# Performance work log

Hardware: AMD Instinct MI355X
Metric: run time of the kernel (lower is better)

Reference implementation:

```python
import jax, jax.numpy as jnp
import numpy as np

D = 1024       # embedding_dim
H = 16         # num_attention_heads
B = 2
S = 2048       # seq_len == context_len


def setup_inputs() -> dict:
    key = jax.random.key(0)
    k1, k2, k3 = jax.random.split(key, 3)
    X = jax.random.normal(k1, (B, S, D), dtype=jnp.float32)
    W_qkv = jax.random.normal(k2, (D, 3 * D), dtype=jnp.float32) * 0.02
    b_qkv = jnp.zeros((3 * D,), dtype=jnp.float32)
    W_out = jax.random.normal(k3, (D, D), dtype=jnp.float32) * 0.02
    b_out = jnp.zeros((D,), dtype=jnp.float32)
    return {"X": X, "W_qkv": W_qkv, "b_qkv": b_qkv, "W_out": W_out, "b_out": b_out}


def reference(X, W_qkv, b_qkv, W_out, b_out):
    b, s, d = X.shape
    hd = d // H
    # fused QKV projection (GPT-2 Conv1D == x @ W + b)
    qkv = X @ W_qkv + b_qkv                       # [b, s, 3d]
    q, k, v = jnp.split(qkv, 3, axis=2)
    # [b, h, s, hd]
    q = q.reshape(b, s, H, hd).transpose(0, 2, 1, 3)
    k = k.reshape(b, s, H, hd).transpose(0, 2, 1, 3)
    v = v.reshape(b, s, H, hd).transpose(0, 2, 1, 3)
    # NOTE: source scales by rsqrt(embedding_dim), not head_dim
    scale = 1.0 / jnp.sqrt(jnp.float32(d))
    scores = jnp.einsum("bhqd,bhkd->bhqk", q, k) * scale
    causal = jnp.tril(jnp.ones((s, s), dtype=bool))
    scores = jnp.where(causal[None, None], scores, -jnp.inf)
    # attention_dropout applied pre-softmax in source; identity at eval (p used here = 0)
    probs = jax.nn.softmax(scores, axis=-1)
    attn = jnp.einsum("bhqk,bhkd->bhqd", probs, v)
    attn = attn.transpose(0, 2, 1, 3).reshape(b, s, d)
    out = attn @ W_out + b_out                    # outwards proj; dropout eval = identity
    return out
```

## Files before the change

kernel.cpp:

```cpp
#include <hip/hip_runtime.h>

#define S_LEN 2048
#define DIM   1024
#define NHEAD 16
#define HDIM  64
#define Q_PRESCALE 0.045084220027780106f

typedef __attribute__((ext_vector_type(8))) short  short8;
typedef __attribute__((ext_vector_type(4))) float  floatx4;
typedef __attribute__((ext_vector_type(4))) unsigned short ushort4v;
typedef __attribute__((ext_vector_type(4))) unsigned int uintx4;

__device__ inline unsigned short f2bf(float f) {
  unsigned v = __builtin_bit_cast(unsigned, f);
  v += 0x7FFFu + ((v >> 16) & 1u);
  return (unsigned short)(v >> 16);
}

__device__ inline unsigned cvt_pk_bf16(float a, float b) {
  unsigned r;
  asm("v_cvt_pk_bf16_f32 %0, %1, %2" : "=v"(r) : "v"(a), "v"(b));
  return r;
}

__device__ inline void permlane16_swap_rw(unsigned &a, unsigned &b) {
  asm("v_permlane16_swap_b32 %0, %1" : "+v"(a), "+v"(b));
}

__device__ inline void async16(const unsigned short* g, unsigned short* l) {
  __builtin_amdgcn_global_load_lds(
      (const __attribute__((address_space(1))) unsigned int*)g,
      (__attribute__((address_space(3))) unsigned int*)l, 16, 0, 0);
}

__global__ __launch_bounds__(256) void prep_kernel(
    const float* __restrict__ X, const float* __restrict__ Wqkv,
    const float* __restrict__ Wout, unsigned short* __restrict__ Xb,
    unsigned short* __restrict__ Wqkvt, unsigned short* __restrict__ Woutt) {
  const int j = blockIdx.x, t = threadIdx.x;
  if (j >= 4096) {
    int i = ((j - 4096) * 256 + t) * 8;
    float4 a = *(const float4*)&X[i];
    float4 b = *(const float4*)&X[i + 4];
    short8 o;
    o[0] = (short)f2bf(a.x); o[1] = (short)f2bf(a.y);
    o[2] = (short)f2bf(a.z); o[3] = (short)f2bf(a.w);
    o[4] = (short)f2bf(b.x); o[5] = (short)f2bf(b.y);
    o[6] = (short)f2bf(b.z); o[7] = (short)f2bf(b.w);
    *(short8*)&Xb[i] = o;
    return;
  }
  __shared__ unsigned short tile[32][33];
  const float* in; unsigned short* out; int N, tn, tk;
  if (j < 3072) { in = Wqkv; out = Wqkvt; N = 3072; tn = j % 96; tk = j / 96; }
  else { int u = j - 3072; in = Wout; out = Woutt; N = 1024; tn = u & 31; tk = u >> 5; }
  const int n0 = tn * 32, k0 = tk * 32;
  const int tx = t & 31, ty = t >> 5;
#pragma unroll
  for (int i = 0; i < 32; i += 8)
    tile[ty + i][tx] = f2bf(in[(size_t)(k0 + ty + i) * N + n0 + tx]);
  __syncthreads();
#pragma unroll
  for (int i = 0; i < 32; i += 8)
    out[(size_t)(n0 + ty + i) * 1024 + k0 + tx] = tile[tx][ty + i];
}

#define GEMM128_BODY(APTR, BPTR)                                                   \
  __shared__ __align__(16) unsigned short As[128][64];                             \
  __shared__ __align__(16) unsigned short Bs[128][64];                             \
  const int m0 = blockIdx.y * 128, n0 = blockIdx.x * 128;                          \
  const int t = threadIdx.x, lane = t & 63, wave = t >> 6;                         \
  const int quad = lane >> 4, l16 = lane & 15;                                     \
  const int wm = (wave >> 1) * 64, wn = (wave & 1) * 64;                           \
  const int lr = lane >> 3, lc = lane & 7, sc8 = (lc ^ lr) * 8;                    \
  const int sw = l16 & 7;                                                          \
  const int pA0 = (quad ^ sw) * 8, pA1 = ((4 + quad) ^ sw) * 8;                    \
  floatx4 acc[4][4];                                                               \
  _Pragma("unroll") for (int mi = 0; mi < 4; mi++)                                 \
      _Pragma("unroll") for (int ni = 0; ni < 4; ni++)                             \
          acc[mi][ni] = (floatx4){0.f, 0.f, 0.f, 0.f};                             \
  for (int k0 = 0; k0 < DIM; k0 += 64) {                                           \
    _Pragma("unroll") for (int i = 0; i < 4; i++) {                                \
      int rb = wave * 32 + i * 8;                                                  \
      async16(&APTR[(size_t)(m0 + rb + lr) * DIM + k0 + sc8], &As[rb][0]);         \
      async16(&BPTR[(size_t)(n0 + rb + lr) * DIM + k0 + sc8], &Bs[rb][0]);         \
    }                                                                              \
    __syncthreads();                                                               \
    short8 a0[4], a1[4];                                                           \
    _Pragma("unroll") for (int mi = 0; mi < 4; mi++) {                             \
      int row = wm + mi * 16 + l16;                                                \
      a0[mi] = *(const short8*)&As[row][pA0];                                      \
      a1[mi] = *(const short8*)&As[row][pA1];                                      \
    }                                                                              \
    _Pragma("unroll") for (int ni = 0; ni < 4; ni++) {                             \
      int row = wn + ni * 16 + l16;                                                \
      short8 b0 = *(const short8*)&Bs[row][pA0];                                   \
      short8 b1 = *(const short8*)&Bs[row][pA1];                                   \
      _Pragma("unroll") for (int mi = 0; mi < 4; mi++) {                           \
        acc[mi][ni] = __builtin_amdgcn_mfma_f32_16x16x32_bf16(a0[mi], b0, acc[mi][ni], 0, 0, 0); \
        acc[mi][ni] = __builtin_amdgcn_mfma_f32_16x16x32_bf16(a1[mi], b1, acc[mi][ni], 0, 0, 0); \
      }                                                                            \
    }                                                                              \
    __syncthreads();                                                               \
  }

__global__ __launch_bounds__(256) void gemm_qkv128(
    const unsigned short* __restrict__ Xb,
    const unsigned short* __restrict__ Wt,
    const float* __restrict__ bias,
    unsigned short* __restrict__ Qg,
    unsigned short* __restrict__ Kg,
    unsigned short* __restrict__ Vgt) {
  GEMM128_BODY(Xb, Wt)
  const int section = n0 >> 10;
  const int head = ((n0 + wn) >> 6) & 15;
#pragma unroll
  for (int mi = 0; mi < 4; mi++) {
    int mg = m0 + wm + mi * 16 + quad * 4;
    int bb = mg >> 11, sb = mg & 2047;
    size_t y = (size_t)bb * NHEAD + head;
    if (section == 2) {
#pragma unroll
      for (int ni = 0; ni < 4; ni++) {
        int hdi = ni * 16 + l16;
        float bv = bias[n0 + wn + hdi];
        ushort4v o;
#pragma unroll
        for (int r = 0; r < 4; r++) o[r] = f2bf(acc[mi][ni][r] + bv);
        *(ushort4v*)&Vgt[(y * HDIM + hdi) * S_LEN + sb] = o;
      }
    } else if (section == 0) {
#pragma unroll
      for (int ni = 0; ni < 4; ni++) {
        int hdi = ni * 16 + l16;
        float bv = bias[n0 + wn + hdi];
#pragma unroll
        for (int r = 0; r < 4; r++)
          Qg[(y * S_LEN + sb + r) * HDIM + hdi] = f2bf((acc[mi][ni][r] + bv) * Q_PRESCALE);
      }
    } else {
#pragma unroll
      for (int ni = 0; ni < 4; ni++) {
        int hdi = ni * 16 + l16;
        float bv = bias[n0 + wn + hdi];
#pragma unroll
        for (int r = 0; r < 4; r++)
          Kg[(y * S_LEN + sb + r) * HDIM + hdi] = f2bf(acc[mi][ni][r] + bv);
      }
    }
  }
}

__global__ __launch_bounds__(128) void gemm_out64(
    const unsigned short* __restrict__ A,
    const unsigned short* __restrict__ Wt,
    const float* __restrict__ bias,
    float* __restrict__ outp) {
  __shared__ __align__(16) unsigned short As[64][64];
  __shared__ __align__(16) unsigned short Bs[64][64];
  const int m0 = blockIdx.y * 64, n0 = blockIdx.x * 64;
  const int t = threadIdx.x, lane = t & 63, wave = t >> 6;
  const int quad = lane >> 4, l16 = lane & 15;
  const int wn = wave * 32;
  const int lr = lane >> 3, lc = lane & 7, sc8 = (lc ^ lr) * 8;
  const int sw = l16 & 7;
  const int pA0 = (quad ^ sw) * 8, pA1 = ((4 + quad) ^ sw) * 8;
  floatx4 acc[4][2];
#pragma unroll
  for (int mi = 0; mi < 4; mi++)
#pragma unroll
    for (int ni = 0; ni < 2; ni++) acc[mi][ni] = (floatx4){0.f, 0.f, 0.f, 0.f};

  for (int k0 = 0; k0 < DIM; k0 += 64) {
#pragma unroll
    for (int i = 0; i < 4; i++) {
      int rb = wave * 32 + i * 8;
      async16(&A[(size_t)(m0 + rb + lr) * DIM + k0 + sc8], &As[rb][0]);
      async16(&Wt[(size_t)(n0 + rb + lr) * DIM + k0 + sc8], &Bs[rb][0]);
    }
    __syncthreads();
    short8 a0[4], a1[4];
#pragma unroll
    for (int mi = 0; mi < 4; mi++) {
      int row = mi * 16 + l16;
      a0[mi] = *(const short8*)&As[row][pA0];
      a1[mi] = *(const short8*)&As[row][pA1];
    }
#pragma unroll
    for (int ni = 0; ni < 2; ni++) {
      int row = wn + ni * 16 + l16;
      short8 b0 = *(const short8*)&Bs[row][pA0];
      short8 b1 = *(const short8*)&Bs[row][pA1];
#pragma unroll
      for (int mi = 0; mi < 4; mi++) {
        acc[mi][ni] = __builtin_amdgcn_mfma_f32_16x16x32_bf16(a0[mi], b0, acc[mi][ni], 0, 0, 0);
        acc[mi][ni] = __builtin_amdgcn_mfma_f32_16x16x32_bf16(a1[mi], b1, acc[mi][ni], 0, 0, 0);
      }
    }
    __syncthreads();
  }
#pragma unroll
  for (int ni = 0; ni < 2; ni++) {
    int n = n0 + wn + ni * 16 + l16;
    float bv = bias[n];
#pragma unroll
    for (int mi = 0; mi < 4; mi++) {
      int mg = m0 + mi * 16 + quad * 4;
#pragma unroll
      for (int r = 0; r < 4; r++)
        outp[(size_t)(mg + r) * DIM + n] = acc[mi][ni][r] + bv;
    }
  }
}

__global__ __launch_bounds__(256) void gemm_qkv_kernel(
    const float* __restrict__ X,
    const unsigned short* __restrict__ Wt,
    const float* __restrict__ bias,
    unsigned short* __restrict__ Qg,
    unsigned short* __restrict__ Kg,
    unsigned short* __restrict__ Vgt,
    int g0, int G) {
  __shared__ __align__(16) unsigned short As[64][72];
  __shared__ __align__(16) unsigned short Bs[64][72];
  const int tn = blockIdx.x;
  const int section = tn / G, within = tn % G;
  const int n0 = section * 1024 + (g0 + within) * 64;
  const int m0 = blockIdx.y * 64;
  const int t = threadIdx.x, lane = t & 63, wave = t >> 6;
  const int quad = lane >> 4, l16 = lane & 15;

  floatx4 acc[4];
#pragma unroll
  for (int i = 0; i < 4; i++) acc[i] = (floatx4){0.f, 0.f, 0.f, 0.f};

  for (int k0 = 0; k0 < DIM; k0 += 64) {
#pragma unroll
    for (int i = 0; i < 2; i++) {
      int v = t + i * 256;
      int row = v >> 3, cc = (v & 7) * 8;
      float4 f0 = *(const float4*)&X[(size_t)(m0 + row) * DIM + k0 + cc];
      float4 f1 = *(const float4*)&X[(size_t)(m0 + row) * DIM + k0 + cc + 4];
      short8 o;
      o[0] = (short)f2bf(f0.x); o[1] = (short)f2bf(f0.y);
      o[2] = (short)f2bf(f0.z); o[3] = (short)f2bf(f0.w);
      o[4] = (short)f2bf(f1.x); o[5] = (short)f2bf(f1.y);
      o[6] = (short)f2bf(f1.z); o[7] = (short)f2bf(f1.w);
      *(short8*)&As[row][cc] = o;
      *(short8*)&Bs[row][cc] = *(const short8*)&Wt[(size_t)(n0 + row) * DIM + k0 + cc];
    }
    __syncthreads();
    short8 a0 = *(const short8*)&As[wave * 16 + l16][quad * 8];
    short8 a1 = *(const short8*)&As[wave * 16 + l16][32 + quad * 8];
#pragma unroll
    for (int nt = 0; nt < 4; nt++) {
      short8 b0 = *(const short8*)&Bs[nt * 16 + l16][quad * 8];
      short8 b1 = *(const short8*)&Bs[nt * 16 + l16][32 + quad * 8];
      acc[nt] = __builtin_amdgcn_mfma_f32_16x16x32_bf16(a0, b0, acc[nt], 0, 0, 0);
      acc[nt] = __builtin_amdgcn_mfma_f32_16x16x32_bf16(a1, b1, acc[nt], 0, 0, 0);
    }
    __syncthreads();
  }

  const int mbase = m0 + wave * 16 + quad * 4;
  const int b = mbase >> 11, sbase = mbase & 2047;
  const int y = b * G + within;
  if (section == 2) {
#pragma unroll
    for (int nt = 0; nt < 4; nt++) {
      int hdi = nt * 16 + l16;
      float bv = bias[n0 + hdi];
      ushort4v o;
#pragma unroll
      for (int r = 0; r < 4; r++) o[r] = f2bf(acc[nt][r] + bv);
      *(ushort4v*)&Vgt[((size_t)y * HDIM + hdi) * S_LEN + sbase] = o;
    }
  } else if (section == 0) {
#pragma unroll
    for (int nt = 0; nt < 4; nt++) {
      int hdi = nt * 16 + l16;
      float bv = bias[n0 + hdi];
#pragma unroll
      for (int r = 0; r < 4; r++)
        Qg[((size_t)y * S_LEN + sbase + r) * HDIM + hdi] =
            f2bf((acc[nt][r] + bv) * Q_PRESCALE);
    }
  } else {
#pragma unroll
    for (int nt = 0; nt < 4; nt++) {
      int hdi = nt * 16 + l16;
      float bv = bias[n0 + hdi];
#pragma unroll
      for (int r = 0; r < 4; r++)
        Kg[((size_t)y * S_LEN + sbase + r) * HDIM + hdi] = f2bf(acc[nt][r] + bv);
    }
  }
}

__global__ __launch_bounds__(256) void attn_kernel(
    const unsigned short* __restrict__ Qg,
    const unsigned short* __restrict__ Kg,
    const unsigned short* __restrict__ Vgt,
    unsigned short* __restrict__ attnB) {
  __shared__ __align__(16) unsigned short Ks[2][64][64];
  __shared__ __align__(16) unsigned short Vs[2][64][64];

  const int y = blockIdx.x;
  const int b = y >> 4, h = y & 15;
  const int qt = 31 - blockIdx.y;
  const int q0 = qt * 64;
  const int nT = qt + 1;
  const int t = threadIdx.x;
  const int lane = t & 63, wave = t >> 6;
  const int quad = lane >> 4, l16 = lane & 15;
  const int lr = lane >> 3, lc = lane & 7;
  const int sc8 = (lc ^ lr) * 8;
  const int sw = l16 & 7;
  const int p0 = (quad ^ sw) * 8, p1 = ((4 + quad) ^ sw) * 8;

  const unsigned short* Qh = Qg + (size_t)y * S_LEN * HDIM;
  const unsigned short* Kh = Kg + (size_t)y * S_LEN * HDIM;
  const unsigned short* Vh = Vgt + (size_t)y * HDIM * S_LEN;

  const unsigned ov = (l16 == 0) ? 0x3F803F80u : 0u;
  const uintx4 ou = {ov, ov, ov, ov};
  const short8 ones = __builtin_bit_cast(short8, ou);

  short8 aq0, aq1;
  {
    const unsigned short* qp = &Qh[(size_t)(q0 + wave * 16 + l16) * HDIM];
    aq0 = *(const short8*)&qp[quad * 8];
    aq1 = *(const short8*)&qp[32 + quad * 8];
  }

  floatx4 o_acc[5];
#pragma unroll
  for (int dt = 0; dt < 5; dt++) o_acc[dt] = (floatx4){0.f, 0.f, 0.f, 0.f};

  {
    int rb = wave * 16;
#pragma unroll
    for (int i = 0; i < 2; i++) {
      async16(&Kh[(size_t)(rb + i * 8 + lr) * HDIM + sc8], &Ks[0][rb + i * 8][0]);
      async16(&Vh[(size_t)(rb + i * 8 + lr) * S_LEN + sc8], &Vs[0][rb + i * 8][0]);
    }
  }

  for (int tt = 0; tt < nT; tt++) {
    const int j0 = tt * 64;
    const int buf = tt & 1;
    __syncthreads();
    if (tt + 1 < nT) {
      int j1 = j0 + 64, nb = 1 - buf;
      int rb = wave * 16;
#pragma unroll
      for (int i = 0; i < 2; i++) {
        async16(&Kh[(size_t)(j1 + rb + i * 8 + lr) * HDIM + sc8], &Ks[nb][rb + i * 8][0]);
        async16(&Vh[(size_t)(rb + i * 8 + lr) * S_LEN + j1 + sc8], &Vs[nb][rb + i * 8][0]);
      }
    }

    floatx4 sc[4];
#pragma unroll
    for (int nt = 0; nt < 4; nt++) {
      short8 kb0 = *(const short8*)&Ks[buf][nt * 16 + l16][p0];
      short8 kb1 = *(const short8*)&Ks[buf][nt * 16 + l16][p1];
      sc[nt] = (floatx4){0.f, 0.f, 0.f, 0.f};
      sc[nt] = __builtin_amdgcn_mfma_f32_16x16x32_bf16(kb0, aq0, sc[nt], 0, 0, 0);
      sc[nt] = __builtin_amdgcn_mfma_f32_16x16x32_bf16(kb1, aq1, sc[nt], 0, 0, 0);
    }

    float p[4][4];
#pragma unroll
    for (int nt = 0; nt < 4; nt++)
#pragma unroll
      for (int r = 0; r < 4; r++)
        p[nt][r] = exp2f(sc[nt][r]);
    if (j0 == q0) {
      const int ql = wave * 16 + l16;
#pragma unroll
      for (int nt = 0; nt < 4; nt++)
#pragma unroll
        for (int r = 0; r < 4; r++)
          if (nt * 16 + quad * 4 + r > ql) p[nt][r] = 0.f;
    }

    unsigned pk00 = cvt_pk_bf16(p[0][0], p[0][1]), pk01 = cvt_pk_bf16(p[0][2], p[0][3]);
    unsigned pk10 = cvt_pk_bf16(p[1][0], p[1][1]), pk11 = cvt_pk_bf16(p[1][2], p[1][3]);
    unsigned pk20 = cvt_pk_bf16(p[2][0], p[2][1]), pk21 = cvt_pk_bf16(p[2][2], p[2][3]);
    unsigned pk30 = cvt_pk_bf16(p[3][0], p[3][1]), pk31 = cvt_pk_bf16(p[3][2], p[3][3]);

    auto sa0 = __builtin_amdgcn_permlane32_swap(pk00, pk10, false, false);
    auto sa1 = __builtin_amdgcn_permlane32_swap(pk01, pk11, false, false);
    auto sb0 = __builtin_amdgcn_permlane32_swap(pk20, pk30, false, false);
    auto sb1 = __builtin_amdgcn_permlane32_swap(pk21, pk31, false, false);
    unsigned xa0 = (unsigned)sa0[0], ya0 = (unsigned)sa0[1];
    unsigned xa1 = (unsigned)sa1[0], ya1 = (unsigned)sa1[1];
    unsigned xb0 = (unsigned)sb0[0], yb0 = (unsigned)sb0[1];
    unsigned xb1 = (unsigned)sb1[0], yb1 = (unsigned)sb1[1];
    permlane16_swap_rw(xa0, ya0);
    permlane16_swap_rw(xa1, ya1);
    permlane16_swap_rw(xb0, yb0);
    permlane16_swap_rw(xb1, yb1);
    uintx4 u0 = {xa0, xa1, ya0, ya1};
    short8 ap0 = __builtin_bit_cast(short8, u0);
    uintx4 u1 = {xb0, xb1, yb0, yb1};
    short8 ap1 = __builtin_bit_cast(short8, u1);

#pragma unroll
    for (int dt = 0; dt < 5; dt++) {
      short8 vb0 = (dt < 4) ? *(const short8*)&Vs[buf][dt * 16 + l16][p0] : ones;
      short8 vb1 = (dt < 4) ? *(const short8*)&Vs[buf][dt * 16 + l16][p1] : ones;
      o_acc[dt] = __builtin_amdgcn_mfma_f32_16x16x32_bf16(ap0, vb0, o_acc[dt], 0, 0, 0);
      o_acc[dt] = __builtin_amdgcn_mfma_f32_16x16x32_bf16(ap1, vb1, o_acc[dt], 0, 0, 0);
    }
  }

  float linv[4];
#pragma unroll
  for (int r = 0; r < 4; r++)
    linv[r] = 1.0f / __shfl(o_acc[4][r], quad << 4);
#pragma unroll
  for (int dt = 0; dt < 4; dt++)
#pragma unroll
    for (int r = 0; r < 4; r++) {
      int qg = q0 + wave * 16 + quad * 4 + r;
      attnB[(size_t)(b * S_LEN + qg) * DIM + h * HDIM + dt * 16 + l16] =
          f2bf(o_acc[dt][r] * linv[r]);
    }
}

extern "C" void kernel_launch(void* const* d_in, const int* in_sizes, int n_in,
                              void* d_out, int out_size, void* d_ws, size_t ws_size,
                              hipStream_t stream) {
  const float* X    = (const float*)d_in[0];
  const float* Wqkv = (const float*)d_in[1];
  const float* bqkv = (const float*)d_in[2];
  const float* Wout = (const float*)d_in[3];
  const float* bout = (const float*)d_in[4];
  float* outp = (float*)d_out;

  unsigned short* Wqkvt = (unsigned short*)d_ws;
  unsigned short* Woutt = Wqkvt + (size_t)3145728;
  unsigned short* attnB = Woutt + (size_t)1048576;
  unsigned short* Qg    = attnB + (size_t)4194304;
  unsigned short* Kg    = Qg + (size_t)4194304;
  unsigned short* Vgt   = Kg + (size_t)4194304;
  unsigned short* Xb    = Vgt + (size_t)4194304;

  const bool bigWs = ws_size >= (size_t)48 * 1024 * 1024;

  if (bigWs) {
    prep_kernel<<<6144, 256, 0, stream>>>(X, Wqkv, Wout, Xb, Wqkvt, Woutt);
    gemm_qkv128<<<dim3(24, 32), 256, 0, stream>>>(Xb, Wqkvt, bqkv, Qg, Kg, Vgt);
  } else {
    prep_kernel<<<4096, 256, 0, stream>>>(X, Wqkv, Wout, nullptr, Wqkvt, Woutt);
    gemm_qkv_kernel<<<dim3(48, 64), 256, 0, stream>>>(
        X, Wqkvt, bqkv, Qg, Kg, Vgt, 0, 16);
  }
  attn_kernel<<<dim3(32, 32), 256, 0, stream>>>(Qg, Kg, Vgt, attnB);
  gemm_out64<<<dim3(16, 64), 128, 0, stream>>>(attnB, Woutt, bout, outp);
}
```

Baseline: 179.6 us.

## Software-pipeline PV MFMA behind next QK^T and store Q transposed

```diff
diff --git a/kernel.cpp b/kernel.cpp
--- a/kernel.cpp
+++ b/kernel.cpp
@@ -108,7 +108,7 @@
     const unsigned short* __restrict__ Xb,
     const unsigned short* __restrict__ Wt,
     const float* __restrict__ bias,
-    unsigned short* __restrict__ Qg,
+    unsigned short* __restrict__ Qgt,
     unsigned short* __restrict__ Kg,
     unsigned short* __restrict__ Vgt) {
   GEMM128_BODY(Xb, Wt)
@@ -134,9 +134,10 @@
       for (int ni = 0; ni < 4; ni++) {
         int hdi = ni * 16 + l16;
         float bv = bias[n0 + wn + hdi];
-#pragma unroll
-        for (int r = 0; r < 4; r++)
-          Qg[(y * S_LEN + sb + r) * HDIM + hdi] = f2bf((acc[mi][ni][r] + bv) * Q_PRESCALE);
+        ushort4v o;
+#pragma unroll
+        for (int r = 0; r < 4; r++) o[r] = f2bf((acc[mi][ni][r] + bv) * Q_PRESCALE);
+        *(ushort4v*)&Qgt[(y * HDIM + hdi) * S_LEN + sb] = o;
       }
     } else {
 #pragma unroll
@@ -217,7 +218,7 @@
     const float* __restrict__ X,
     const unsigned short* __restrict__ Wt,
     const float* __restrict__ bias,
-    unsigned short* __restrict__ Qg,
+    unsigned short* __restrict__ Qgt,
     unsigned short* __restrict__ Kg,
     unsigned short* __restrict__ Vgt,
     int g0, int G) {
@@ -280,10 +281,10 @@
     for (int nt = 0; nt < 4; nt++) {
       int hdi = nt * 16 + l16;
       float bv = bias[n0 + hdi];
-#pragma unroll
-      for (int r = 0; r < 4; r++)
-        Qg[((size_t)y * S_LEN + sbase + r) * HDIM + hdi] =
-            f2bf((acc[nt][r] + bv) * Q_PRESCALE);
+      ushort4v o;
+#pragma unroll
+      for (int r = 0; r < 4; r++) o[r] = f2bf((acc[nt][r] + bv) * Q_PRESCALE);
+      *(ushort4v*)&Qgt[((size_t)y * HDIM + hdi) * S_LEN + sbase] = o;
     }
   } else {
 #pragma unroll
@@ -298,12 +299,12 @@
 }
 
 __global__ __launch_bounds__(256) void attn_kernel(
-    const unsigned short* __restrict__ Qg,
+    const unsigned short* __restrict__ Qgt,
     const unsigned short* __restrict__ Kg,
     const unsigned short* __restrict__ Vgt,
     unsigned short* __restrict__ attnB) {
   __shared__ __align__(16) unsigned short Ks[2][64][64];
-  __shared__ __align__(16) unsigned short Vs[2][64][64];
+  __shared__ __align__(16) unsigned short Vs[3][64][64];
 
   const int y = blockIdx.x;
   const int b = y >> 4, h = y & 15;
@@ -318,7 +319,7 @@
   const int sw = l16 & 7;
   const int p0 = (quad ^ sw) * 8, p1 = ((4 + quad) ^ sw) * 8;
 
-  const unsigned short* Qh = Qg + (size_t)y * S_LEN * HDIM;
+  const unsigned short* Qh = Qgt + (size_t)y * S_LEN * HDIM;
   const unsigned short* Kh = Kg + (size_t)y * S_LEN * HDIM;
   const unsigned short* Vh = Vgt + (size_t)y * HDIM * S_LEN;
 
@@ -328,9 +329,12 @@
 
   short8 aq0, aq1;
   {
-    const unsigned short* qp = &Qh[(size_t)(q0 + wave * 16 + l16) * HDIM];
-    aq0 = *(const short8*)&qp[quad * 8];
-    aq1 = *(const short8*)&qp[32 + quad * 8];
+    const int s = q0 + wave * 16 + l16;
+#pragma unroll
+    for (int j = 0; j < 8; j++) {
+      aq0[j] = (short)Qh[(size_t)(quad * 8 + j) * S_LEN + s];
+      aq1[j] = (short)Qh[(size_t)(32 + quad * 8 + j) * S_LEN + s];
+    }
   }
 
   floatx4 o_acc[5];
@@ -346,28 +350,41 @@
     }
   }
 
+  int prevV = 2, curV = 0, nextV = 1;
+  short8 apP0, apP1;
+
   for (int tt = 0; tt < nT; tt++) {
     const int j0 = tt * 64;
-    const int buf = tt & 1;
+    const int kb = tt & 1;
     __syncthreads();
     if (tt + 1 < nT) {
-      int j1 = j0 + 64, nb = 1 - buf;
+      int j1 = j0 + 64;
       int rb = wave * 16;
 #pragma unroll
       for (int i = 0; i < 2; i++) {
-        async16(&Kh[(size_t)(j1 + rb + i * 8 + lr) * HDIM + sc8], &Ks[nb][rb + i * 8][0]);
-        async16(&Vh[(size_t)(rb + i * 8 + lr) * S_LEN + j1 + sc8], &Vs[nb][rb + i * 8][0]);
+        async16(&Kh[(size_t)(j1 + rb + i * 8 + lr) * HDIM + sc8], &Ks[kb ^ 1][rb + i * 8][0]);
+        async16(&Vh[(size_t)(rb + i * 8 + lr) * S_LEN + j1 + sc8], &Vs[nextV][rb + i * 8][0]);
       }
     }
 
     floatx4 sc[4];
 #pragma unroll
     for (int nt = 0; nt < 4; nt++) {
-      short8 kb0 = *(const short8*)&Ks[buf][nt * 16 + l16][p0];
-      short8 kb1 = *(const short8*)&Ks[buf][nt * 16 + l16][p1];
+      short8 kb0 = *(const short8*)&Ks[kb][nt * 16 + l16][p0];
+      short8 kb1 = *(const short8*)&Ks[kb][nt * 16 + l16][p1];
       sc[nt] = (floatx4){0.f, 0.f, 0.f, 0.f};
       sc[nt] = __builtin_amdgcn_mfma_f32_16x16x32_bf16(kb0, aq0, sc[nt], 0, 0, 0);
       sc[nt] = __builtin_amdgcn_mfma_f32_16x16x32_bf16(kb1, aq1, sc[nt], 0, 0, 0);
+    }
+
+    if (tt > 0) {
+#pragma unroll
+      for (int dt = 0; dt < 5; dt++) {
+        short8 vb0 = (dt < 4) ? *(const short8*)&Vs[prevV][dt * 16 + l16][p0] : ones;
+        short8 vb1 = (dt < 4) ? *(const short8*)&Vs[prevV][dt * 16 + l16][p1] : ones;
+        o_acc[dt] = __builtin_amdgcn_mfma_f32_16x16x32_bf16(apP0, vb0, o_acc[dt], 0, 0, 0);
+        o_acc[dt] = __builtin_amdgcn_mfma_f32_16x16x32_bf16(apP1, vb1, o_acc[dt], 0, 0, 0);
+      }
     }
 
     float p[4][4];
@@ -403,17 +420,19 @@
     permlane16_swap_rw(xb0, yb0);
     permlane16_swap_rw(xb1, yb1);
     uintx4 u0 = {xa0, xa1, ya0, ya1};
-    short8 ap0 = __builtin_bit_cast(short8, u0);
+    apP0 = __builtin_bit_cast(short8, u0);
     uintx4 u1 = {xb0, xb1, yb0, yb1};
-    short8 ap1 = __builtin_bit_cast(short8, u1);
-
-#pragma unroll
-    for (int dt = 0; dt < 5; dt++) {
-      short8 vb0 = (dt < 4) ? *(const short8*)&Vs[buf][dt * 16 + l16][p0] : ones;
-      short8 vb1 = (dt < 4) ? *(const short8*)&Vs[buf][dt * 16 + l16][p1] : ones;
-      o_acc[dt] = __builtin_amdgcn_mfma_f32_16x16x32_bf16(ap0, vb0, o_acc[dt], 0, 0, 0);
-      o_acc[dt] = __builtin_amdgcn_mfma_f32_16x16x32_bf16(ap1, vb1, o_acc[dt], 0, 0, 0);
-    }
+    apP1 = __builtin_bit_cast(short8, u1);
+
+    int tmp = prevV; prevV = curV; curV = nextV; nextV = tmp;
+  }
+
+#pragma unroll
+  for (int dt = 0; dt < 5; dt++) {
+    short8 vb0 = (dt < 4) ? *(const short8*)&Vs[prevV][dt * 16 + l16][p0] : ones;
+    short8 vb1 = (dt < 4) ? *(const short8*)&Vs[prevV][dt * 16 + l16][p1] : ones;
+    o_acc[dt] = __builtin_amdgcn_mfma_f32_16x16x32_bf16(apP0, vb0, o_acc[dt], 0, 0, 0);
+    o_acc[dt] = __builtin_amdgcn_mfma_f32_16x16x32_bf16(apP1, vb1, o_acc[dt], 0, 0, 0);
   }
 
   float linv[4];
@@ -443,8 +462,8 @@
   unsigned short* Wqkvt = (unsigned short*)d_ws;
   unsigned short* Woutt = Wqkvt + (size_t)3145728;
   unsigned short* attnB = Woutt + (size_t)1048576;
-  unsigned short* Qg    = attnB + (size_t)4194304;
-  unsigned short* Kg    = Qg + (size_t)4194304;
+  unsigned short* Qgt   = attnB + (size_t)4194304;
+  unsigned short* Kg    = Qgt + (size_t)4194304;
   unsigned short* Vgt   = Kg + (size_t)4194304;
   unsigned short* Xb    = Vgt + (size_t)4194304;
 
@@ -452,12 +471,12 @@
 
   if (bigWs) {
     prep_kernel<<<6144, 256, 0, stream>>>(X, Wqkv, Wout, Xb, Wqkvt, Woutt);
-    gemm_qkv128<<<dim3(24, 32), 256, 0, stream>>>(Xb, Wqkvt, bqkv, Qg, Kg, Vgt);
+    gemm_qkv128<<<dim3(24, 32), 256, 0, stream>>>(Xb, Wqkvt, bqkv, Qgt, Kg, Vgt);
   } else {
     prep_kernel<<<4096, 256, 0, stream>>>(X, Wqkv, Wout, nullptr, Wqkvt, Woutt);
     gemm_qkv_kernel<<<dim3(48, 64), 256, 0, stream>>>(
-        X, Wqkvt, bqkv, Qg, Kg, Vgt, 0, 16);
-  }
-  attn_kernel<<<dim3(32, 32), 256, 0, stream>>>(Qg, Kg, Vgt, attnB);
+        X, Wqkvt, bqkv, Qgt, Kg, Vgt, 0, 16);
+  }
+  attn_kernel<<<dim3(32, 32), 256, 0, stream>>>(Qgt, Kg, Vgt, attnB);
   gemm_out64<<<dim3(16, 64), 128, 0, stream>>>(attnB, Woutt, bout, outp);
 }
```

After: 179.8 us. About the same (+0.1%).
